# Optimization experiments

Measured on AMD Instinct MI355X. Metric: run time of the kernel, lower is better.

Reference implementation:

```python
import jax, jax.numpy as jnp
import numpy as np

N_NODES = 190464      # 1024 graphs * 186 nodes (62 channels * 3 bands)
N_EDGES = 3047424     # avg degree 16
F_IN = 5
HEADS = 4
C_OUT = 24
NODES_PER_GRAPH = 186


def setup_inputs() -> dict:
    key = jax.random.key(0)
    ks = jax.random.split(key, 8)
    x = jax.random.normal(ks[0], (N_NODES, F_IN), dtype=jnp.float32)
    edge_index = jax.random.randint(ks[1], (2, N_EDGES), 0, N_NODES, dtype=jnp.int64)
    batch = (jnp.arange(N_NODES, dtype=jnp.int64) // NODES_PER_GRAPH)
    # learned parameters
    bn_gamma = jnp.ones((F_IN,), jnp.float32)
    bn_beta = jnp.zeros((F_IN,), jnp.float32)
    lin_w = jax.random.normal(ks[2], (HEADS * C_OUT, F_IN), jnp.float32) * (1.0 / np.sqrt(F_IN))
    att_src = jax.random.normal(ks[3], (HEADS, C_OUT), jnp.float32) * 0.1
    att_dst = jax.random.normal(ks[4], (HEADS, C_OUT), jnp.float32) * 0.1
    gat_bias = jnp.zeros((C_OUT,), jnp.float32)
    conv_w = jax.random.normal(ks[5], (8, C_OUT, 62), jnp.float32) * 0.05  # Conv1d(24->8,k=62)
    conv_b = jnp.zeros((8,), jnp.float32)
    return {"x": x, "edge_index": edge_index, "batch": batch,
            "bn_gamma": bn_gamma, "bn_beta": bn_beta, "lin_w": lin_w,
            "att_src": att_src, "att_dst": att_dst, "gat_bias": gat_bias,
            "conv_w": conv_w, "conv_b": conv_b}


def reference(x, edge_index, batch, bn_gamma, bn_beta, lin_w, att_src, att_dst,
              gat_bias, conv_w, conv_b):
    N = x.shape[0]
    H, C = att_src.shape
    B = N // NODES_PER_GRAPH  # batch.max()+1, known statically

    # BatchNorm1d (training-mode batch statistics, eps=1e-5)
    mu = x.mean(0)
    var = x.var(0)
    xn = (x - mu) * jax.lax.rsqrt(var + 1e-5) * bn_gamma + bn_beta

    # GATConv (PyG defaults: add_self_loops=True, negative_slope=0.2,
    # concat=False -> mean over heads; dropout inactive at eval)
    loop = jnp.arange(N, dtype=edge_index.dtype)
    src = jnp.concatenate([edge_index[0], loop])
    dst = jnp.concatenate([edge_index[1], loop])

    h = (xn @ lin_w.T).reshape(N, H, C)            # [N,H,C]
    a_src = jnp.einsum('nhc,hc->nh', h, att_src)   # [N,H]
    a_dst = jnp.einsum('nhc,hc->nh', h, att_dst)

    logits = jax.nn.leaky_relu(a_src[src] + a_dst[dst], 0.2)   # [E+N,H]
    m = jax.ops.segment_max(logits, dst, num_segments=N)       # per-dst softmax
    e = jnp.exp(logits - m[dst])
    denom = jax.ops.segment_sum(e, dst, num_segments=N)
    attn = e / (denom[dst] + 1e-16)

    out = jax.ops.segment_sum(h[src] * attn[:, :, None], dst, num_segments=N)
    out = out.mean(axis=1) + gat_bias              # concat=False -> head mean
    out = jax.nn.elu(out)                          # [N,24]

    y = out.reshape(B, NODES_PER_GRAPH, C).transpose(0, 2, 1)  # [B,24,186]
    y = jax.lax.conv_general_dilated(y, conv_w, window_strides=(1,),
                                     padding='VALID',
                                     dimension_numbers=('NCH', 'OIH', 'NCH'))
    y = y + conv_b[None, :, None]                  # [B,8,125]
    return jax.nn.leaky_relu(y, 0.01)
```

## Files before the change

kernel.cpp:

```cpp
#include <hip/hip_runtime.h>
#include <hip/hip_bf16.h>
#include <math.h>

#define N_NODES 190464
#define NPG 186
#define NGRAPH 1024
#define CAP 4096
#define NPART 8
#define PCAP 512
#define KW 62
#define OCH 8
#define TOUT 125
#define BCHUNK 4096
#define NBLK 744

#define SWZ(p) ((p) ^ ((((p) >> 5) & 3) << 2))

typedef _Float16 h2 __attribute__((ext_vector_type(2)));

#if __has_builtin(__builtin_amdgcn_fdot2)
#define FDOT2(a, b, c) __builtin_amdgcn_fdot2((a), (b), (c), false)
#else
#define FDOT2(a, b, c) ((c) + (float)(a).x * (float)(b).x + (float)(a).y * (float)(b).y)
#endif

__device__ __forceinline__ h2 bc_h2(unsigned u) {
    union { unsigned u; h2 h; } v; v.u = u; return v.h;
}
__device__ __forceinline__ unsigned pk_h2(float a, float b) {
    union { h2 h; unsigned u; } v;
    v.h = h2{(_Float16)a, (_Float16)b};
    return v.u;
}

__device__ __forceinline__ float lrelu2(float v) { return v > 0.f ? v : 0.2f * v; }

__global__ __launch_bounds__(256) void bn_stats(const float* __restrict__ x,
                                                double* __restrict__ pstats) {
    __shared__ double red[10][4];
    int tid = threadIdx.x;
    int t = blockIdx.x * 256 + tid;
    const float4* xv = (const float4*)x + (size_t)t * 5;
    float4 v0 = xv[0], v1 = xv[1], v2 = xv[2], v3 = xv[3], v4 = xv[4];

    float s[5], ss[5];
    s[0] = v0.x + v1.y + v2.z + v3.w;
    s[1] = v0.y + v1.z + v2.w + v4.x;
    s[2] = v0.z + v1.w + v3.x + v4.y;
    s[3] = v0.w + v2.x + v3.y + v4.z;
    s[4] = v1.x + v2.y + v3.z + v4.w;
    ss[0] = v0.x * v0.x + v1.y * v1.y + v2.z * v2.z + v3.w * v3.w;
    ss[1] = v0.y * v0.y + v1.z * v1.z + v2.w * v2.w + v4.x * v4.x;
    ss[2] = v0.z * v0.z + v1.w * v1.w + v3.x * v3.x + v4.y * v4.y;
    ss[3] = v0.w * v0.w + v2.x * v2.x + v3.y * v3.y + v4.z * v4.z;
    ss[4] = v1.x * v1.x + v2.y * v2.y + v3.z * v3.z + v4.w * v4.w;

    double sd[5], ssd[5];
#pragma unroll
    for (int f = 0; f < 5; ++f) { sd[f] = (double)s[f]; ssd[f] = (double)ss[f]; }
#pragma unroll
    for (int f = 0; f < 5; ++f) {
        for (int off = 32; off; off >>= 1) {
            sd[f] += __shfl_down(sd[f], off);
            ssd[f] += __shfl_down(ssd[f], off);
        }
    }
    if ((tid & 63) == 0) {
        int w = tid >> 6;
#pragma unroll
        for (int f = 0; f < 5; ++f) { red[f][w] = sd[f]; red[5 + f][w] = ssd[f]; }
    }
    __syncthreads();
    if (tid < 10)
        pstats[tid * 256 + blockIdx.x] =
            red[tid][0] + red[tid][1] + red[tid][2] + red[tid][3];
}

__global__ void prep(const double* __restrict__ pstats,
                     const float* __restrict__ gamma,
                     const float* __restrict__ beta,
                     const float* __restrict__ lin_w,
                     const float* __restrict__ att_src,
                     const float* __restrict__ att_dst,
                     const float* __restrict__ conv_w,
                     float* __restrict__ prm,
                     unsigned* __restrict__ whu) {
    __shared__ double fstats[10];
    __shared__ float scale[5], shift[5];
    int t = threadIdx.x;
    int w = t >> 6, l = t & 63;
    for (int f = w; f < 10; f += 4) {
        const double* p = pstats + f * 256;
        double v = p[l] + p[l + 64] + p[l + 128] + p[l + 192];
        for (int off = 32; off; off >>= 1) v += __shfl_down(v, off);
        if (l == 0) fstats[f] = v;
    }
    __syncthreads();
    if (t < 5) {
        double mu = fstats[t] / (double)N_NODES;
        double var = fstats[5 + t] / (double)N_NODES - mu * mu;
        double rstd = 1.0 / sqrt(var + 1e-5);
        float sc = (float)rstd * gamma[t];
        scale[t] = sc;
        shift[t] = beta[t] - (float)mu * sc;
    }
    __syncthreads();
    if (t < 96) {
        float hbv = 0.f;
#pragma unroll
        for (int f = 0; f < 5; ++f) {
            float ww = lin_w[t * 5 + f];
            prm[t * 5 + f] = ww * scale[f];
            hbv += ww * shift[f];
        }
        prm[480 + t] = hbv;
    }
    __syncthreads();
    if (t < 8) {
        int h = t & 3;
        const float* att = (t < 4) ? att_src : att_dst;
        int wb = (t < 4) ? 576 : 600;
        int bb = (t < 4) ? 596 : 620;
        float bsum = 0.f;
        float wsum[5] = {0, 0, 0, 0, 0};
        for (int c = 0; c < 24; ++c) {
            float a = att[h * 24 + c];
            int o = h * 24 + c;
#pragma unroll
            for (int f = 0; f < 5; ++f) wsum[f] += a * prm[o * 5 + f];
            bsum += a * prm[480 + o];
        }
#pragma unroll
        for (int f = 0; f < 5; ++f) prm[wb + h * 5 + f] = wsum[f];
        prm[bb + h] = bsum;
    }
    for (int idx = t; idx < OCH * 24 * 32; idx += 256) {
        int j = idx & 31, oc = idx >> 5;
        const float* wr = conv_w + oc * KW;
        int k0 = 2 * j, k1 = 2 * j + 1, km = 2 * j - 1;
        float e0 = (k0 < KW) ? wr[k0] : 0.f;
        float e1 = (k1 < KW) ? wr[k1] : 0.f;
        float s0 = (km >= 0 && km < KW) ? wr[km] : 0.f;
        float s1 = e0;
        whu[idx * 2 + 0] = pk_h2(e0, e1);
        whu[idx * 2 + 1] = pk_h2(s0, s1);
    }
}

__global__ __launch_bounds__(256) void bucket_pairs(const int* __restrict__ ei,
                                                    const int E,
                                                    int* __restrict__ gcnt,
                                                    unsigned* __restrict__ pairbuf) {
    __shared__ int h[NGRAPH];
    int tid = threadIdx.x;
    int p = blockIdx.x & (NPART - 1);
    int e0 = blockIdx.x * BCHUNK;
#pragma unroll
    for (int i = tid; i < NGRAPH; i += 256) h[i] = 0;
    __syncthreads();
    for (int i = tid; i < BCHUNK; i += 256) {
        int dst = ei[E + e0 + i];
        unsigned g = (unsigned)dst / NPG;
        atomicAdd(&h[g], 1);
    }
    __syncthreads();
    int* gc = gcnt + p * NGRAPH;
    for (int g = tid; g < NGRAPH; g += 256) {
        int c = h[g];
        h[g] = c ? atomicAdd(&gc[g], c) : 0;
    }
    __syncthreads();
    for (int i = tid; i < BCHUNK; i += 256) {
        int src = ei[e0 + i];
        int dst = ei[E + e0 + i];
        unsigned g = (unsigned)dst / NPG;
        int dloc = dst - (int)g * NPG;
        int pos = atomicAdd(&h[g], 1);
        if (pos < PCAP)
            pairbuf[(size_t)g * CAP + p * PCAP + pos] =
                (unsigned)src | ((unsigned)dloc << 18);
    }
}

__global__ __launch_bounds__(256) void gat_sort(
    const unsigned* __restrict__ pairbuf, const int* __restrict__ gcnt,
    int* __restrict__ rpg, int* __restrict__ lsrcg) {
    __shared__ int deg[188];
    __shared__ int cur[188];
    int g = blockIdx.x, tid = threadIdx.x;
    if (tid < 188) deg[tid] = 0;
    __syncthreads();
    for (int p = 0; p < NPART; ++p) {
        int ne = min(gcnt[p * NGRAPH + g], PCAP);
        const unsigned* pb = pairbuf + (size_t)g * CAP + p * PCAP;
        for (int i = tid; i < ne; i += 256) atomicAdd(&deg[pb[i] >> 18], 1);
    }
    __syncthreads();
    if (tid < 64) {
        int base = tid * 3;
        int d0 = (base < NPG) ? deg[base] : 0;
        int d1 = (base + 1 < NPG) ? deg[base + 1] : 0;
        int d2 = (base + 2 < NPG) ? deg[base + 2] : 0;
        int tsum = d0 + d1 + d2;
        int run = tsum;
        for (int off = 1; off < 64; off <<= 1) {
            int u = __shfl_up(run, off);
            if (tid >= off) run += u;
        }
        int excl = run - tsum;
        int* rp = rpg + (size_t)g * 188;
        if (base < NPG)     { rp[base] = excl;              cur[base] = excl; }
        if (base + 1 < NPG) { rp[base + 1] = excl + d0;     cur[base + 1] = excl + d0; }
        if (base + 2 < NPG) { rp[base + 2] = excl + d0 + d1; cur[base + 2] = excl + d0 + d1; }
        if (tid == 63) rp[NPG] = run;
    }
    __syncthreads();
    int* ls = lsrcg + (size_t)g * CAP;
    for (int p = 0; p < NPART; ++p) {
        int ne = min(gcnt[p * NGRAPH + g], PCAP);
        const unsigned* pb = pairbuf + (size_t)g * CAP + p * PCAP;
        for (int i = tid; i < ne; i += 256) {
            unsigned e = pb[i];
            int pos = atomicAdd(&cur[e >> 18], 1);
            ls[pos] = (int)(e & 0x3FFFFu);
        }
    }
}

__global__ __launch_bounds__(256) void gat_compute(
    const int* __restrict__ rpg, const int* __restrict__ lsrcg,
    const float* __restrict__ x, const float* __restrict__ prm,
    const float* __restrict__ gat_bias, float* __restrict__ gout) {
    __shared__ float prms[624];
    __shared__ float gb[24];
    int tid = threadIdx.x;
    for (int i = tid; i < 624; i += 256) prms[i] = prm[i];
    if (tid < 24) gb[tid] = gat_bias[tid];
    __syncthreads();

    int t = blockIdx.x * 256 + tid;
    int n = t >> 2, h = t & 3;
    if (n >= N_NODES) return;
    int g = n / NPG;
    int nl = n - g * NPG;
    const int* rp = rpg + (size_t)g * 188;
    int beg = rp[nl], end = rp[nl + 1];
    const int* ls = lsrcg + (size_t)g * CAP;

    float aw[5], dw[5];
#pragma unroll
    for (int f = 0; f < 5; ++f) {
        aw[f] = prms[576 + h * 5 + f];
        dw[f] = prms[600 + h * 5 + f];
    }
    float ab = prms[596 + h], db = prms[620 + h];

    const float* xn = x + (size_t)n * 5;
    float4 xd4 = *(const float4*)xn;
    float xd5 = xn[4];
    float ad = db + dw[0] * xd4.x + dw[1] * xd4.y + dw[2] * xd4.z +
               dw[3] * xd4.w + dw[4] * xd5;
    float as = ab + aw[0] * xd4.x + aw[1] * xd4.y + aw[2] * xd4.z +
               aw[3] * xd4.w + aw[4] * xd5;
    float e = __expf(lrelu2(as + ad));
    float denom = e;
    float ax[5];
    ax[0] = e * xd4.x; ax[1] = e * xd4.y; ax[2] = e * xd4.z;
    ax[3] = e * xd4.w; ax[4] = e * xd5;

    int i = beg;
    for (; i + 1 < end; i += 2) {
        int s0 = ls[i], s1 = ls[i + 1];
        const float* p0 = x + (size_t)s0 * 5;
        const float* p1 = x + (size_t)s1 * 5;
        float4 a4 = *(const float4*)p0;
        float a5 = p0[4];
        float4 b4 = *(const float4*)p1;
        float b5 = p1[4];
        float l0 = ab + aw[0] * a4.x + aw[1] * a4.y + aw[2] * a4.z +
                   aw[3] * a4.w + aw[4] * a5;
        float l1 = ab + aw[0] * b4.x + aw[1] * b4.y + aw[2] * b4.z +
                   aw[3] * b4.w + aw[4] * b5;
        float e0 = __expf(lrelu2(l0 + ad));
        float e1 = __expf(lrelu2(l1 + ad));
        denom += e0 + e1;
        ax[0] += e0 * a4.x + e1 * b4.x;
        ax[1] += e0 * a4.y + e1 * b4.y;
        ax[2] += e0 * a4.z + e1 * b4.z;
        ax[3] += e0 * a4.w + e1 * b4.w;
        ax[4] += e0 * a5 + e1 * b5;
    }
    if (i < end) {
        int s0 = ls[i];
        const float* p0 = x + (size_t)s0 * 5;
        float4 a4 = *(const float4*)p0;
        float a5 = p0[4];
        float l0 = ab + aw[0] * a4.x + aw[1] * a4.y + aw[2] * a4.z +
                   aw[3] * a4.w + aw[4] * a5;
        float e0 = __expf(lrelu2(l0 + ad));
        denom += e0;
        ax[0] += e0 * a4.x; ax[1] += e0 * a4.y; ax[2] += e0 * a4.z;
        ax[3] += e0 * a4.w; ax[4] += e0 * a5;
    }

    float inv = 1.f / (denom + 1e-16f);
#pragma unroll
    for (int f = 0; f < 5; ++f) ax[f] *= inv;
    float* go = gout + (size_t)n * 24;
#pragma unroll
    for (int c = 0; c < 24; ++c) {
        int o = h * 24 + c;
        float vv = prms[480 + o];
#pragma unroll
        for (int f = 0; f < 5; ++f) vv += prms[o * 5 + f] * ax[f];
        vv *= 0.25f;
        vv += __shfl_xor(vv, 1);
        vv += __shfl_xor(vv, 2);
        if ((c & 3) == h) {
            vv += gb[c];
            go[c] = vv > 0.f ? vv : expm1f(vv);
        }
    }
}

__global__ __launch_bounds__(256) void conv_k(
    const float* __restrict__ gat, const unsigned* __restrict__ whu,
    const float* __restrict__ b, float* __restrict__ out) {
    __shared__ float it32[24 * 196];
    __shared__ unsigned ite[24 * 96];
    __shared__ unsigned wshu[4 * 24 * 64];
    int bid = blockIdx.x;
    int g = bid >> 1;
    int oh = (bid & 1) * 4;
    int tid = threadIdx.x;

    for (int i = tid; i < NPG * 24; i += 256) {
        int p = i / 24, c = i % 24;
        it32[c * 196 + SWZ(p)] = gat[(size_t)g * (NPG * 24) + i];
    }
    for (int i = tid; i < 24 * 6; i += 256) {
        int c = i / 6, p = 186 + (i % 6);
        it32[c * 196 + SWZ(p)] = 0.f;
    }
    for (int i = tid; i < 4 * 24 * 64; i += 256)
        wshu[i] = whu[(size_t)oh * 24 * 64 + i];
    __syncthreads();
    for (int i = tid; i < 24 * 96; i += 256) {
        int c = i / 96, p2 = i - c * 96;
        float f0 = it32[c * 196 + SWZ(2 * p2)];
        float f1 = it32[c * 196 + SWZ(2 * p2 + 1)];
        ite[i] = pk_h2(f0, f1);
    }
    __syncthreads();

    int hw = tid >> 5;
    int ol = hw & 3;
    int rh = hw >> 2;
    int tt = tid & 31;

    float a0 = 0.f, a1 = 0.f, a2 = 0.f, a3 = 0.f;
#pragma unroll
    for (int r = 0; r < 12; ++r) {
        int i = rh * 12 + r;
        const unsigned* pe = &ite[i * 96 + 2 * tt];
        const uint4* wr4 = (const uint4*)&wshu[(ol * 24 + i) * 64];
        uint2 cur = *(const uint2*)pe;
#pragma unroll
        for (int jj = 0; jj < 16; ++jj) {
            uint2 nxt = *(const uint2*)(pe + 2 * (jj + 1));
            uint4 wv = wr4[jj];
            h2 ew0 = bc_h2(wv.x), sw0 = bc_h2(wv.y);
            h2 ew1 = bc_h2(wv.z), sw1 = bc_h2(wv.w);
            h2 px = bc_h2(cur.x), py = bc_h2(cur.y), nx = bc_h2(nxt.x);
            a0 = FDOT2(ew0, px, a0);
            a1 = FDOT2(sw0, px, a1);
            a2 = FDOT2(ew0, py, a2);
            a3 = FDOT2(sw0, py, a3);
            a0 = FDOT2(ew1, py, a0);
            a1 = FDOT2(sw1, py, a1);
            a2 = FDOT2(ew1, nx, a2);
            a3 = FDOT2(sw1, nx, a3);
            cur = nxt;
        }
    }
    __syncthreads();
    float* part = (float*)wshu;
    int t0 = tt * 4;
    *(float4*)&part[hw * 128 + t0] = make_float4(a0, a1, a2, a3);
    __syncthreads();
    for (int idx = tid; idx < 4 * TOUT; idx += 256) {
        int o = idx / TOUT, t = idx - o * TOUT;
        float s = part[o * 128 + t] + part[(4 + o) * 128 + t] + b[oh + o];
        out[((size_t)g * OCH + oh + o) * TOUT + t] = s > 0.f ? s : 0.01f * s;
    }
}

extern "C" void kernel_launch(void* const* d_in, const int* in_sizes, int n_in,
                              void* d_out, int out_size, void* d_ws, size_t ws_size,
                              hipStream_t stream) {
    const float* x        = (const float*)d_in[0];
    const int*   ei       = (const int*)d_in[1];
    const float* bn_gamma = (const float*)d_in[3];
    const float* bn_beta  = (const float*)d_in[4];
    const float* lin_w    = (const float*)d_in[5];
    const float* att_src  = (const float*)d_in[6];
    const float* att_dst  = (const float*)d_in[7];
    const float* gat_bias = (const float*)d_in[8];
    const float* conv_w   = (const float*)d_in[9];
    const float* conv_b   = (const float*)d_in[10];
    float* out = (float*)d_out;
    float* wsf = (float*)d_ws;
    int*   wsi = (int*)d_ws;

    const int E = in_sizes[1] / 2;

    int*      gcnt    = wsi;
    double*   pstats  = (double*)(wsf + 8192);
    float*    prm     = wsf + 13312;
    unsigned* whu     = (unsigned*)(wsi + 13936);
    int*      rpg     = wsi + 26224;
    unsigned* pairbuf = (unsigned*)(rpg + (size_t)NGRAPH * 188);
    int*      lsrcg   = (int*)(pairbuf + (size_t)NGRAPH * CAP);
    float*    gout    = (float*)(lsrcg + (size_t)NGRAPH * CAP);

    (void)hipMemsetAsync(d_ws, 0, 13312 * 4, stream);

    bn_stats<<<186, 256, 0, stream>>>(x, pstats);
    prep<<<1, 256, 0, stream>>>(pstats, bn_gamma, bn_beta, lin_w,
                                att_src, att_dst, conv_w, prm, whu);
    bucket_pairs<<<NBLK, 256, 0, stream>>>(ei, E, gcnt, pairbuf);
    gat_sort<<<NGRAPH, 256, 0, stream>>>(pairbuf, gcnt, rpg, lsrcg);
    gat_compute<<<(N_NODES * 4) / 256, 256, 0, stream>>>(rpg, lsrcg, x, prm,
                                                         gat_bias, gout);
    conv_k<<<NGRAPH * 2, 256, 0, stream>>>(gout, whu, conv_b, out);
}
```

Measured before the change: 170.1 us.

## Split edges across the four lanes per node instead of heads

```diff
diff --git a/kernel.cpp b/kernel.cpp
--- a/kernel.cpp
+++ b/kernel.cpp
@@ -239,7 +239,7 @@
     __syncthreads();
 
     int t = blockIdx.x * 256 + tid;
-    int n = t >> 2, h = t & 3;
+    int n = t >> 2, l = t & 3;
     if (n >= N_NODES) return;
     int g = n / NPG;
     int nl = n - g * NPG;
@@ -247,76 +247,97 @@
     int beg = rp[nl], end = rp[nl + 1];
     const int* ls = lsrcg + (size_t)g * CAP;
 
-    float aw[5], dw[5];
-#pragma unroll
-    for (int f = 0; f < 5; ++f) {
-        aw[f] = prms[576 + h * 5 + f];
-        dw[f] = prms[600 + h * 5 + f];
-    }
-    float ab = prms[596 + h], db = prms[620 + h];
+    float aw[4][5], ab[4];
+#pragma unroll
+    for (int h = 0; h < 4; ++h) {
+        ab[h] = prms[596 + h];
+#pragma unroll
+        for (int f = 0; f < 5; ++f) aw[h][f] = prms[576 + h * 5 + f];
+    }
 
     const float* xn = x + (size_t)n * 5;
     float4 xd4 = *(const float4*)xn;
     float xd5 = xn[4];
-    float ad = db + dw[0] * xd4.x + dw[1] * xd4.y + dw[2] * xd4.z +
-               dw[3] * xd4.w + dw[4] * xd5;
-    float as = ab + aw[0] * xd4.x + aw[1] * xd4.y + aw[2] * xd4.z +
-               aw[3] * xd4.w + aw[4] * xd5;
-    float e = __expf(lrelu2(as + ad));
-    float denom = e;
-    float ax[5];
-    ax[0] = e * xd4.x; ax[1] = e * xd4.y; ax[2] = e * xd4.z;
-    ax[3] = e * xd4.w; ax[4] = e * xd5;
-
-    int i = beg;
-    for (; i + 1 < end; i += 2) {
-        int s0 = ls[i], s1 = ls[i + 1];
-        const float* p0 = x + (size_t)s0 * 5;
-        const float* p1 = x + (size_t)s1 * 5;
-        float4 a4 = *(const float4*)p0;
-        float a5 = p0[4];
-        float4 b4 = *(const float4*)p1;
-        float b5 = p1[4];
-        float l0 = ab + aw[0] * a4.x + aw[1] * a4.y + aw[2] * a4.z +
-                   aw[3] * a4.w + aw[4] * a5;
-        float l1 = ab + aw[0] * b4.x + aw[1] * b4.y + aw[2] * b4.z +
-                   aw[3] * b4.w + aw[4] * b5;
-        float e0 = __expf(lrelu2(l0 + ad));
-        float e1 = __expf(lrelu2(l1 + ad));
-        denom += e0 + e1;
-        ax[0] += e0 * a4.x + e1 * b4.x;
-        ax[1] += e0 * a4.y + e1 * b4.y;
-        ax[2] += e0 * a4.z + e1 * b4.z;
-        ax[3] += e0 * a4.w + e1 * b4.w;
-        ax[4] += e0 * a5 + e1 * b5;
-    }
-    if (i < end) {
-        int s0 = ls[i];
-        const float* p0 = x + (size_t)s0 * 5;
-        float4 a4 = *(const float4*)p0;
-        float a5 = p0[4];
-        float l0 = ab + aw[0] * a4.x + aw[1] * a4.y + aw[2] * a4.z +
-                   aw[3] * a4.w + aw[4] * a5;
-        float e0 = __expf(lrelu2(l0 + ad));
-        denom += e0;
-        ax[0] += e0 * a4.x; ax[1] += e0 * a4.y; ax[2] += e0 * a4.z;
-        ax[3] += e0 * a4.w; ax[4] += e0 * a5;
-    }
-
-    float inv = 1.f / (denom + 1e-16f);
-#pragma unroll
-    for (int f = 0; f < 5; ++f) ax[f] *= inv;
+    float xd[5] = {xd4.x, xd4.y, xd4.z, xd4.w, xd5};
+    float ad[4];
+#pragma unroll
+    for (int h = 0; h < 4; ++h) {
+        float v = prms[620 + h];
+#pragma unroll
+        for (int f = 0; f < 5; ++f) v += prms[600 + h * 5 + f] * xd[f];
+        ad[h] = v;
+    }
+
+    float ax[4][5], den[4];
+#pragma unroll
+    for (int h = 0; h < 4; ++h) {
+        den[h] = 0.f;
+#pragma unroll
+        for (int f = 0; f < 5; ++f) ax[h][f] = 0.f;
+    }
+    if (l == 0) {
+#pragma unroll
+        for (int h = 0; h < 4; ++h) {
+            float as = ab[h];
+#pragma unroll
+            for (int f = 0; f < 5; ++f) as += aw[h][f] * xd[f];
+            float e = __expf(lrelu2(as + ad[h]));
+            den[h] += e;
+#pragma unroll
+            for (int f = 0; f < 5; ++f) ax[h][f] += e * xd[f];
+        }
+    }
+    for (int i = beg + l; i < end; i += 4) {
+        int s = ls[i];
+        const float* xp = x + (size_t)s * 5;
+        float4 a4 = *(const float4*)xp;
+        float a5 = xp[4];
+        float xs[5] = {a4.x, a4.y, a4.z, a4.w, a5};
+#pragma unroll
+        for (int h = 0; h < 4; ++h) {
+            float lg = ab[h];
+#pragma unroll
+            for (int f = 0; f < 5; ++f) lg += aw[h][f] * xs[f];
+            float e = __expf(lrelu2(lg + ad[h]));
+            den[h] += e;
+#pragma unroll
+            for (int f = 0; f < 5; ++f) ax[h][f] += e * xs[f];
+        }
+    }
+#pragma unroll
+    for (int h = 0; h < 4; ++h) {
+        den[h] += __shfl_xor(den[h], 1);
+        den[h] += __shfl_xor(den[h], 2);
+#pragma unroll
+        for (int f = 0; f < 5; ++f) {
+            ax[h][f] += __shfl_xor(ax[h][f], 1);
+            ax[h][f] += __shfl_xor(ax[h][f], 2);
+        }
+    }
+    float axs[5] = {0, 0, 0, 0, 0};
+    float dn = 0.f;
+#pragma unroll
+    for (int hh = 0; hh < 4; ++hh) {
+        if (l == hh) {
+            dn = den[hh];
+#pragma unroll
+            for (int f = 0; f < 5; ++f) axs[f] = ax[hh][f];
+        }
+    }
+    float inv = 1.f / (dn + 1e-16f);
+#pragma unroll
+    for (int f = 0; f < 5; ++f) axs[f] *= inv;
     float* go = gout + (size_t)n * 24;
 #pragma unroll
     for (int c = 0; c < 24; ++c) {
-        int o = h * 24 + c;
+        int o = l * 24 + c;
         float vv = prms[480 + o];
 #pragma unroll
-        for (int f = 0; f < 5; ++f) vv += prms[o * 5 + f] * ax[f];
+        for (int f = 0; f < 5; ++f) vv += prms[o * 5 + f] * axs[f];
         vv *= 0.25f;
         vv += __shfl_xor(vv, 1);
         vv += __shfl_xor(vv, 2);
-        if ((c & 3) == h) {
+        if ((c & 3) == l) {
             vv += gb[c];
             go[c] = vv > 0.f ? vv : expm1f(vv);
         }
```

After: 174.3 us. 1.02x slower.
